# Performance work log

Hardware: AMD Instinct MI355X
Metric: run time of the kernel (lower is better)

The kernel has to match this reference:

```python
import jax, jax.numpy as jnp
import numpy as np
from jax import lax

EDGE_THRESHOLD = 0.1
DILATION_SIZE = 5
VAR_RATIO_THRESHOLD = 2.0
LOCAL_WINDOW = 7

SOBEL_X = jnp.array([[-1., 0., 1.], [-2., 0., 2.], [-1., 0., 1.]], dtype=jnp.float32)[None, None]
SOBEL_Y = jnp.array([[-1., -2., -1.], [0., 0., 0.], [1., 2., 1.]], dtype=jnp.float32)[None, None]


def _conv_same(x, k):
    # x: (B,1,H,W), k: (1,1,kh,kw), stride 1, SAME padding (odd kernels)
    return lax.conv_general_dilated(x, k.astype(x.dtype), (1, 1), 'SAME',
                                    dimension_numbers=('NCHW', 'OIHW', 'NCHW'))


def _rgb_to_luminance(x):
    w = jnp.array([0.299, 0.587, 0.114], dtype=x.dtype).reshape(1, 3, 1, 1)
    return (x * w).sum(axis=1, keepdims=True)


def _sobel_edge(lum):
    gx = _conv_same(lum, SOBEL_X)
    gy = _conv_same(lum, SOBEL_Y)
    return jnp.sqrt(gx * gx + gy * gy + 1e-12)


def _local_variance(x, mask):
    ws = LOCAL_WINDOW
    ones_k = jnp.ones((1, 1, ws, ws), dtype=x.dtype)
    local_sum = _conv_same(x * mask, ones_k)
    local_cnt = jnp.clip(_conv_same(mask, ones_k), 1.0, None)
    local_mean = local_sum / local_cnt
    local_sq_sum = _conv_same(x * x * mask, ones_k)
    local_var = jnp.clip(local_sq_sum / local_cnt - local_mean ** 2, 0.0, None) * mask
    total = jnp.clip(mask.sum(axis=(2, 3)), 1.0, None)  # (B,1)
    return local_var.sum(axis=(2, 3)) / total  # (B,1)


def _compute_ringing_mask(img):
    lum = _rgb_to_luminance(img) if img.shape[1] == 3 else img
    grad_mag = _sobel_edge(lum)
    E = (grad_mag > EDGE_THRESHOLD).astype(lum.dtype)
    # morphological dilation via max pool, kernel=5, stride=1, SAME padding
    E_dilated = lax.reduce_window(E, -jnp.inf, lax.max,
                                  (1, 1, DILATION_SIZE, DILATION_SIZE),
                                  (1, 1, 1, 1), 'SAME')
    M_prox = jnp.clip(E_dilated - E, 0.0, None)
    M_bg = 1.0 - E_dilated
    var_prox = _local_variance(lum, M_prox)  # (B,1)
    var_bg = _local_variance(lum, M_bg)      # (B,1)
    ratio = var_prox / (var_bg + 1e-12)
    is_ringing = (ratio > VAR_RATIO_THRESHOLD).astype(lum.dtype)  # (B,1)
    return M_prox * is_ringing[:, :, None, None]


def setup_inputs() -> dict:
    key = jax.random.key(0)
    k1, k2 = jax.random.split(key)
    B, C, H, W = 16, 3, 512, 512
    ref = jax.random.uniform(k1, (B, C, H, W), dtype=jnp.float32)
    tgt = jax.random.uniform(k2, (B, C, H, W), dtype=jnp.float32)
    return {"ref": ref, "tgt": tgt}


def reference(ref, tgt):
    ringing_ref = _compute_ringing_mask(ref)
    ringing_tgt = _compute_ringing_mask(tgt)
    return jnp.clip(ringing_tgt - ringing_ref, 0.0, None)
```

## Files before the change

kernel.cpp:

```cpp
#include <hip/hip_runtime.h>

#define HH 512
#define WW 512
#define NPIX (HH*WW)
#define BATCH 16
#define NIMG 32

typedef unsigned char uchar;
typedef unsigned long long u64;

__global__ __launch_bounds__(256) void k_lum(const float4* __restrict__ ref,
                                             const float4* __restrict__ tgt,
                                             float4* __restrict__ lum) {
    int idx = blockIdx.x * 256 + threadIdx.x;
    int img = idx >> 16;
    int p4 = idx & 65535;
    const float4* src = (img < BATCH) ? (ref + (size_t)img * 3 * 65536)
                                      : (tgt + (size_t)(img - BATCH) * 3 * 65536);
    float4 r = src[p4];
    float4 g = src[65536 + p4];
    float4 b = src[131072 + p4];
    float4 o;
    o.x = 0.299f * r.x + 0.587f * g.x + 0.114f * b.x;
    o.y = 0.299f * r.y + 0.587f * g.y + 0.114f * b.y;
    o.z = 0.299f * r.z + 0.587f * g.z + 0.114f * b.z;
    o.w = 0.299f * r.w + 0.587f * g.w + 0.114f * b.w;
    lum[idx] = o;
}


__inline__ __device__ float wave_reduce(float v) {
#pragma unroll
    for (int o = 32; o > 0; o >>= 1) v += __shfl_down(v, o);
    return v;
}

__global__ __launch_bounds__(256) void k_strip(const float* __restrict__ lum,
                                               uchar* __restrict__ Mo_g,
                                               double* __restrict__ acc) {
    int lane = threadIdx.x & 63;
    int gw = blockIdx.x * 4 + (threadIdx.x >> 6);
    int img = gw / 160;
    int rem = gw - img * 160;
    int sy = rem / 10;
    int sx = rem - sy * 10;
    int r0 = sy << 5;
    int c0 = sx * 52;
    int col = c0 + lane - 6;
    bool colok = (unsigned)col < WW;

    int lm1 = (lane > 0) ? lane - 1 : 0;
    int lp1 = (lane < 63) ? lane + 1 : 63;
    int lm2 = (lane > 1) ? lane - 2 : 0;
    int lp2 = (lane < 62) ? lane + 2 : 63;

    const float* Lp = lum + (size_t)img * NPIX;
    uchar* Mo = Mo_g + (size_t)img * NPIX;

    float tm0 = 0, tm1 = 0, tm2 = 0, tm3 = 0;
    float tc0 = 0, tc1 = 0, tc2 = 0, tc3 = 0;
    float tp0 = 0, tp1 = 0, tp2 = 0, tp3 = 0;
    unsigned eb = 0, hb = 0, pbm = 0, vbm = 0;

    float preA = (((unsigned)(r0 - 6) < HH) && colok) ? Lp[(size_t)(r0 - 6) * WW + col] : 0.0f;
    float preB = (((unsigned)(r0 - 5) < HH) && colok) ? Lp[(size_t)(r0 - 5) * WW + col] : 0.0f;

#define LOADROW(Lr) { \
    tm0 = tm1; tc0 = tc1; tp0 = tp1; \
    tm1 = tm2; tc1 = tc2; tp1 = tp2; \
    tm2 = tm3; tc2 = tc3; tp2 = tp3; \
    float ln = preA; preA = preB; \
    { int rr = (Lr) + 2; \
      preB = (((unsigned)rr < HH) && colok) ? Lp[(size_t)rr * WW + col] : 0.0f; } \
    tc3 = ln; tm3 = __shfl(ln, lm1); tp3 = __shfl(ln, lp1); }

#define SOBEL_E(Lr) { \
    float gx = (tp1 - tm1) + 2.0f * (tp2 - tm2) + (tp3 - tm3); \
    float gy = (tm3 + 2.0f * tc3 + tp3) - (tm1 + 2.0f * tc1 + tp1); \
    float grad = sqrtf(gx * gx + gy * gy + 1e-12f); \
    bool e = (grad > 0.1f) && colok && ((unsigned)((Lr) - 1) < HH); \
    u64 ebal = __ballot(e); \
    eb = (eb << 1) | (e ? 1u : 0u); \
    unsigned hE5 = (unsigned)((ebal << 2) >> lane) & 0x1Fu; \
    hb = (hb << 1) | (hE5 ? 1u : 0u); }

    for (int q = 0; q < 2; ++q) { int Lr = r0 - 6 + q; LOADROW(Lr); }
    for (int q = 0; q < 4; ++q) { int Lr = r0 - 4 + q; LOADROW(Lr); SOBEL_E(Lr); }

    float r1p[7], r2p[7], r1v[7], r2v[7];
    unsigned rcn[7];
    unsigned cnt_acc = 0;
    float a1p = 0, a2p = 0, a1v = 0, a2v = 0;
    float c0a = 0, c1a = 0, c2a = 0, c3a = 0;

    for (int o6 = 0; o6 < 6; ++o6) {
#pragma unroll
        for (int u = 0; u < 7; ++u) {
            int j = o6 * 7 + u;
            int Lr = r0 + j;
            LOADROW(Lr);
            SOBEL_E(Lr);
            int m = Lr - 3;
            bool ed = (hb & 0x1Fu) != 0;
            bool e3 = ((eb >> 2) & 1u) != 0;
            bool mrowok = (unsigned)m < HH;
            bool pp = ed && !e3 && mrowok && colok;
            bool vv = (!ed) && mrowok && colok;
            u64 pb = __ballot(pp);
            u64 vb = __ballot(vv);
            pbm = (pbm << 1) | (pp ? 1u : 0u);
            vbm = (vbm << 1) | (vv ? 1u : 0u);

            float xx0 = __shfl(tm0, lm2);
            float xx1 = __shfl(tc0, lm2);
            float xx2 = tm0;
            float xx3 = tc0;
            float xx4 = tp0;
            float xx5 = __shfl(tc0, lp2);
            float xx6 = __shfl(tp0, lp2);
            unsigned pw = (unsigned)((pb << 3) >> lane) & 0x7Fu;
            unsigned vw = (unsigned)((vb << 3) >> lane) & 0x7Fu;
            unsigned cnt_new = (unsigned)__popc(pw) | ((unsigned)__popc(vw) << 8);
            float s1p = 0, s2p = 0, s1v = 0, s2v = 0;
#define TAP(i, xi) { float xq = (xi) * (xi); \
            s1p += ((pw >> (i)) & 1u) ? (xi) : 0.0f; \
            s2p += ((pw >> (i)) & 1u) ? xq : 0.0f; \
            s1v += ((vw >> (i)) & 1u) ? (xi) : 0.0f; \
            s2v += ((vw >> (i)) & 1u) ? xq : 0.0f; }
            TAP(0, xx0) TAP(1, xx1) TAP(2, xx2) TAP(3, xx3)
            TAP(4, xx4) TAP(5, xx5) TAP(6, xx6)
#undef TAP

            if (j >= 7) {
                cnt_acc -= rcn[u];
                a1p -= r1p[u]; a2p -= r2p[u]; a1v -= r1v[u]; a2v -= r2v[u];
            }
            cnt_acc += cnt_new;
            a1p += s1p; a2p += s2p; a1v += s1v; a2v += s2v;
            rcn[u] = cnt_new; r1p[u] = s1p; r2p[u] = s2p; r1v[u] = s1v; r2v[u] = s2v;

            if (j >= 3 && j <= 34) {
                if (lane >= 6 && lane <= 57 && colok)
                    Mo[(size_t)m * WW + col] = (uchar)(pp ? 1 : 0);
            }
            if (j >= 6 && j <= 37) {
                float mp0 = (float)((pbm >> 3) & 1u);
                float mb0 = (float)((vbm >> 3) & 1u);
                if (lane < 6 || lane > 57) { mp0 = 0.0f; mb0 = 0.0f; }
                float cpf = (float)(cnt_acc & 0xFFu);
                float cvf = (float)((cnt_acc >> 8) & 0xFFu);
                float rCp = __builtin_amdgcn_rcpf(fmaxf(cpf, 1.0f));
                float meanp = a1p * rCp;
                float varp = fmaxf(a2p * rCp - meanp * meanp, 0.0f);
                float rCb = __builtin_amdgcn_rcpf(fmaxf(cvf, 1.0f));
                float meanb = a1v * rCb;
                float varb = fmaxf(a2v * rCb - meanb * meanb, 0.0f);
                c0a += varp * mp0; c1a += mp0;
                c2a += varb * mb0; c3a += mb0;
            }
        }
    }

    c0a = wave_reduce(c0a); c1a = wave_reduce(c1a);
    c2a = wave_reduce(c2a); c3a = wave_reduce(c3a);
    if (lane == 0) {
        atomicAdd(&acc[img * 4 + 0], (double)c0a);
        atomicAdd(&acc[img * 4 + 1], (double)c1a);
        atomicAdd(&acc[img * 4 + 2], (double)c2a);
        atomicAdd(&acc[img * 4 + 3], (double)c3a);
    }
}

__global__ void k_flags(const double* __restrict__ acc, float* __restrict__ flags) {
    int i = threadIdx.x;
    if (i >= NIMG) return;
    const double* a = acc + (size_t)i * 4;
    double vp = a[0] / fmax(a[1], 1.0);
    double vb = a[2] / fmax(a[3], 1.0);
    flags[i] = ((vp / (vb + 1e-12)) > 2.0) ? 1.0f : 0.0f;
}

__global__ __launch_bounds__(256) void k_out(const uchar4* __restrict__ M,
                                             const float* __restrict__ flags,
                                             float4* __restrict__ out) {
    int idx = blockIdx.x * 256 + threadIdx.x;
    int b = idx >> 16;
    int p = idx & 65535;
    float fr = flags[b], ft = flags[b + BATCH];
    uchar4 mr = M[(size_t)b * 65536 + p];
    uchar4 mt = M[(size_t)(b + BATCH) * 65536 + p];
    float4 o;
    o.x = fmaxf((mt.x ? ft : 0.0f) - (mr.x ? fr : 0.0f), 0.0f);
    o.y = fmaxf((mt.y ? ft : 0.0f) - (mr.y ? fr : 0.0f), 0.0f);
    o.z = fmaxf((mt.z ? ft : 0.0f) - (mr.z ? fr : 0.0f), 0.0f);
    o.w = fmaxf((mt.w ? ft : 0.0f) - (mr.w ? fr : 0.0f), 0.0f);
    out[idx] = o;
}

extern "C" void kernel_launch(void* const* d_in, const int* in_sizes, int n_in,
                              void* d_out, int out_size, void* d_ws, size_t ws_size,
                              hipStream_t stream) {
    const float* ref = (const float*)d_in[0];
    const float* tgt = (const float*)d_in[1];
    float* out = (float*)d_out;

    char* ws = (char*)d_ws;
    double* acc = (double*)ws;
    float* flags = (float*)(ws + 1024);
    float* lum = (float*)(ws + 2048);
    uchar* Mo = (uchar*)(ws + 2048 + (size_t)NIMG * NPIX * 4);

    (void)hipMemsetAsync(acc, 0, NIMG * 4 * sizeof(double), stream);

    int nAll = NIMG * NPIX;
    k_lum<<<nAll / 4 / 256, 256, 0, stream>>>((const float4*)ref, (const float4*)tgt, (float4*)lum);
    k_strip<<<1280, 256, 0, stream>>>(lum, Mo, acc);
    k_flags<<<1, 64, 0, stream>>>(acc, flags);
    k_out<<<BATCH * NPIX / 4 / 256, 256, 0, stream>>>((const uchar4*)Mo, flags, (float4*)out);
}
```

Baseline: 223.6 us.

## Store luminance in zero-padded buffer and replace lane shuffles with direct loads

Luminance is written into a 544x544 zero-padded layout, so the strip kernel can read neighbour columns and rows directly without bounds checks. Cross-lane shuffles for the Sobel and variance-window taps become extra global/cache loads that are software-prefetched one row ahead. The tap accumulation is also rewritten to use FMAs. The cost is an extra memset of the whole padded buffer on every call (about 38 MB) and more load instructions per row.

```diff
diff --git a/kernel.cpp b/kernel.cpp
--- a/kernel.cpp
+++ b/kernel.cpp
@@ -5,6 +5,8 @@
 #define NPIX (HH*WW)
 #define BATCH 16
 #define NIMG 32
+#define PW 544
+#define PAD 16
 
 typedef unsigned char uchar;
 typedef unsigned long long u64;
@@ -15,6 +17,8 @@
     int idx = blockIdx.x * 256 + threadIdx.x;
     int img = idx >> 16;
     int p4 = idx & 65535;
+    int y = p4 >> 7;
+    int x4 = p4 & 127;
     const float4* src = (img < BATCH) ? (ref + (size_t)img * 3 * 65536)
                                       : (tgt + (size_t)(img - BATCH) * 3 * 65536);
     float4 r = src[p4];
@@ -25,7 +29,7 @@
     o.y = 0.299f * r.y + 0.587f * g.y + 0.114f * b.y;
     o.z = 0.299f * r.z + 0.587f * g.z + 0.114f * b.z;
     o.w = 0.299f * r.w + 0.587f * g.w + 0.114f * b.w;
-    lum[idx] = o;
+    lum[(size_t)img * (PW * PW / 4) + (size_t)(y + PAD) * (PW / 4) + (PAD / 4) + x4] = o;
 }
 
 
@@ -35,7 +39,7 @@
     return v;
 }
 
-__global__ __launch_bounds__(256) void k_strip(const float* __restrict__ lum,
+__global__ __launch_bounds__(256) void k_strip(const float* __restrict__ lum_p,
                                                uchar* __restrict__ Mo_g,
                                                double* __restrict__ acc) {
     int lane = threadIdx.x & 63;
@@ -49,12 +53,8 @@
     int col = c0 + lane - 6;
     bool colok = (unsigned)col < WW;
 
-    int lm1 = (lane > 0) ? lane - 1 : 0;
-    int lp1 = (lane < 63) ? lane + 1 : 63;
-    int lm2 = (lane > 1) ? lane - 2 : 0;
-    int lp2 = (lane < 62) ? lane + 2 : 63;
-
-    const float* Lp = lum + (size_t)img * NPIX;
+    const float* LB = lum_p + (size_t)img * (PW * PW) + (size_t)PAD * PW + PAD;
+    const float* base0 = LB + col;
     uchar* Mo = Mo_g + (size_t)img * NPIX;
 
     float tm0 = 0, tm1 = 0, tm2 = 0, tm3 = 0;
@@ -62,17 +62,9 @@
     float tp0 = 0, tp1 = 0, tp2 = 0, tp3 = 0;
     unsigned eb = 0, hb = 0, pbm = 0, vbm = 0;
 
-    float preA = (((unsigned)(r0 - 6) < HH) && colok) ? Lp[(size_t)(r0 - 6) * WW + col] : 0.0f;
-    float preB = (((unsigned)(r0 - 5) < HH) && colok) ? Lp[(size_t)(r0 - 5) * WW + col] : 0.0f;
-
-#define LOADROW(Lr) { \
-    tm0 = tm1; tc0 = tc1; tp0 = tp1; \
-    tm1 = tm2; tc1 = tc2; tp1 = tp2; \
-    tm2 = tm3; tc2 = tc3; tp2 = tp3; \
-    float ln = preA; preA = preB; \
-    { int rr = (Lr) + 2; \
-      preB = (((unsigned)rr < HH) && colok) ? Lp[(size_t)rr * WW + col] : 0.0f; } \
-    tc3 = ln; tm3 = __shfl(ln, lm1); tp3 = __shfl(ln, lp1); }
+#define SHIFT3() { tm0 = tm1; tc0 = tc1; tp0 = tp1; \
+                   tm1 = tm2; tc1 = tc2; tp1 = tp2; \
+                   tm2 = tm3; tc2 = tc3; tp2 = tp3; }
 
 #define SOBEL_E(Lr) { \
     float gx = (tp1 - tm1) + 2.0f * (tp2 - tm2) + (tp3 - tm3); \
@@ -84,8 +76,27 @@
     unsigned hE5 = (unsigned)((ebal << 2) >> lane) & 0x1Fu; \
     hb = (hb << 1) | (hE5 ? 1u : 0u); }
 
-    for (int q = 0; q < 2; ++q) { int Lr = r0 - 6 + q; LOADROW(Lr); }
-    for (int q = 0; q < 4; ++q) { int Lr = r0 - 4 + q; LOADROW(Lr); SOBEL_E(Lr); }
+    const float* pN = base0 + (ptrdiff_t)r0 * PW;
+    float cA = pN[-1], cB = pN[0], cC = pN[1];
+    const float* pM0 = pN - 3 * PW;
+    float cx0 = pM0[-3], cx1 = pM0[-2], cx5 = pM0[2], cx6 = pM0[3];
+    pN += PW;
+
+    {
+        const float* pR = base0 + (ptrdiff_t)(r0 - 6) * PW;
+        for (int q = 0; q < 2; ++q) {
+            SHIFT3();
+            tm3 = pR[-1]; tc3 = pR[0]; tp3 = pR[1];
+            pR += PW;
+        }
+        for (int q = 0; q < 4; ++q) {
+            int Lr = r0 - 4 + q;
+            SHIFT3();
+            tm3 = pR[-1]; tc3 = pR[0]; tp3 = pR[1];
+            pR += PW;
+            SOBEL_E(Lr);
+        }
+    }
 
     float r1p[7], r2p[7], r1v[7], r2v[7];
     unsigned rcn[7];
@@ -98,8 +109,15 @@
         for (int u = 0; u < 7; ++u) {
             int j = o6 * 7 + u;
             int Lr = r0 + j;
-            LOADROW(Lr);
+
+            float nA = pN[-1], nB = pN[0], nC = pN[1];
+            const float* pM = pN - 3 * PW;
+            float nx0 = pM[-3], nx1 = pM[-2], nx5 = pM[2], nx6 = pM[3];
+
+            SHIFT3();
+            tm3 = cA; tc3 = cB; tp3 = cC;
             SOBEL_E(Lr);
+
             int m = Lr - 3;
             bool ed = (hb & 0x1Fu) != 0;
             bool e3 = ((eb >> 2) & 1u) != 0;
@@ -111,22 +129,22 @@
             pbm = (pbm << 1) | (pp ? 1u : 0u);
             vbm = (vbm << 1) | (vv ? 1u : 0u);
 
-            float xx0 = __shfl(tm0, lm2);
-            float xx1 = __shfl(tc0, lm2);
+            float xx0 = cx0;
+            float xx1 = cx1;
             float xx2 = tm0;
             float xx3 = tc0;
             float xx4 = tp0;
-            float xx5 = __shfl(tc0, lp2);
-            float xx6 = __shfl(tp0, lp2);
+            float xx5 = cx5;
+            float xx6 = cx6;
             unsigned pw = (unsigned)((pb << 3) >> lane) & 0x7Fu;
             unsigned vw = (unsigned)((vb << 3) >> lane) & 0x7Fu;
             unsigned cnt_new = (unsigned)__popc(pw) | ((unsigned)__popc(vw) << 8);
             float s1p = 0, s2p = 0, s1v = 0, s2v = 0;
-#define TAP(i, xi) { float xq = (xi) * (xi); \
-            s1p += ((pw >> (i)) & 1u) ? (xi) : 0.0f; \
-            s2p += ((pw >> (i)) & 1u) ? xq : 0.0f; \
-            s1v += ((vw >> (i)) & 1u) ? (xi) : 0.0f; \
-            s2v += ((vw >> (i)) & 1u) ? xq : 0.0f; }
+#define TAP(i, xi) { \
+            float pxi = ((pw >> (i)) & 1u) ? (xi) : 0.0f; \
+            float vxi = ((vw >> (i)) & 1u) ? (xi) : 0.0f; \
+            s1p += pxi; s2p = fmaf(pxi, (xi), s2p); \
+            s1v += vxi; s2v = fmaf(vxi, (xi), s2v); }
             TAP(0, xx0) TAP(1, xx1) TAP(2, xx2) TAP(3, xx3)
             TAP(4, xx4) TAP(5, xx5) TAP(6, xx6)
 #undef TAP
@@ -158,6 +176,10 @@
                 c0a += varp * mp0; c1a += mp0;
                 c2a += varb * mb0; c3a += mb0;
             }
+
+            cA = nA; cB = nB; cC = nC;
+            cx0 = nx0; cx1 = nx1; cx5 = nx5; cx6 = nx6;
+            pN += PW;
         }
     }
 
@@ -208,9 +230,11 @@
     double* acc = (double*)ws;
     float* flags = (float*)(ws + 1024);
     float* lum = (float*)(ws + 2048);
-    uchar* Mo = (uchar*)(ws + 2048 + (size_t)NIMG * NPIX * 4);
+    size_t lum_bytes = (size_t)NIMG * PW * PW * 4;
+    uchar* Mo = (uchar*)(ws + 2048 + lum_bytes);
 
     (void)hipMemsetAsync(acc, 0, NIMG * 4 * sizeof(double), stream);
+    (void)hipMemsetAsync(lum, 0, lum_bytes, stream);
 
     int nAll = NIMG * NPIX;
     k_lum<<<nAll / 4 / 256, 256, 0, stream>>>((const float4*)ref, (const float4*)tgt, (float4*)lum);
```

Result: slower. 232.3 us (+3.9%).
